# Kernel optimization log

Measured on AMD Instinct MI355X. Metric: run time of the kernel, lower is better.

Reference implementation:

```python
import jax, jax.numpy as jnp
import numpy as np


def _xnor_quant_weight(w):
    # XnorBinaryLinear.quant_weight: row-center, sign-binarize, scale by
    # per-output-channel mean absolute value (STE in training; forward value
    # is sign(wc) * scale).
    wc = w - jnp.mean(w, axis=1, keepdims=True)          # [OC, IC]
    scale = jnp.mean(jnp.abs(wc), axis=1, keepdims=True)  # [OC, 1]
    return jnp.sign(wc) * scale


def setup_inputs() -> dict:
    key = jax.random.key(0)
    k1, k2, k3, k4 = jax.random.split(key, 4)
    OC = IC = 4096
    N_OUT = int(0.05 * IC)  # 204 outlier columns
    TOKENS = 4096
    x = jax.random.normal(k1, (TOKENS, IC), dtype=jnp.float32)
    weight = jax.random.normal(k2, (OC, IC), dtype=jnp.float32) * 0.02
    bias = jax.random.normal(k3, (OC,), dtype=jnp.float32) * 0.02
    outlier_weight = jax.random.normal(k4, (OC, N_OUT), dtype=jnp.float32) * 0.02
    outlier_columns_index = jnp.arange(N_OUT, dtype=jnp.int32)
    return {
        "x": x,
        "weight": weight,
        "bias": bias,
        "outlier_weight": outlier_weight,
        "outlier_columns_index": outlier_columns_index,
    }


def reference(x, weight, bias, outlier_weight, outlier_columns_index):
    # binarize_except_outliers: quantize dense weight, then overwrite the
    # outlier input-channel columns with the kept full-precision weights.
    wq = _xnor_quant_weight(weight)                      # [OC, IC]
    wq = wq.at[:, outlier_columns_index].set(outlier_weight)
    # F.linear(x, w, b) = x @ w.T + b
    return jnp.einsum("ti,oi->to", x, wq) + bias
```

## Files before the change

kernel.cpp:

```cpp
#include <hip/hip_runtime.h>

typedef __bf16 bf16;
typedef __bf16 bf16x8 __attribute__((ext_vector_type(8)));
typedef float  f32x4  __attribute__((ext_vector_type(4)));
typedef float  f32x16 __attribute__((ext_vector_type(16)));
typedef int    i32x4  __attribute__((ext_vector_type(4)));
typedef int    i32x16 __attribute__((ext_vector_type(16)));
typedef signed char i8;

#define OC_N   4096
#define IC_K   4096
#define TOKENS 4096
#define KC     256

__global__ __launch_bounds__(256) void prep_kernel(
    const float* __restrict__ w, const float* __restrict__ x,
    const float* __restrict__ ow, const int* __restrict__ idx,
    i8* __restrict__ wsgn, i8* __restrict__ xq,
    bf16* __restrict__ xo, bf16* __restrict__ wcorr,
    float* __restrict__ scale_arr, float* __restrict__ sx_arr, int n_out)
{
    __shared__ float red[8];
    const int row = blockIdx.x;
    const int t = threadIdx.x;
    const int lane = t & 63, wv = t >> 6;

    const float4* wr = (const float4*)(w + (size_t)row * IC_K);
    const float4* xr = (const float4*)(x + (size_t)row * IC_K);
    float4 v[4], u[4];
#pragma unroll
    for (int i = 0; i < 4; i++) v[i] = wr[i * 256 + t];
#pragma unroll
    for (int i = 0; i < 4; i++) u[i] = xr[i * 256 + t];

    float xg = 0.f, wg = 0.f, og = 0.f;
    if (t < n_out) {
        const int colg = idx[t];
        xg = x[(size_t)row * IC_K + colg];
        wg = w[(size_t)row * IC_K + colg];
        og = ow[(size_t)row * n_out + t];
    }

    float s = 0.f;
#pragma unroll
    for (int i = 0; i < 4; i++)
        s += v[i].x + v[i].y + v[i].z + v[i].w;
    for (int o = 32; o > 0; o >>= 1) s += __shfl_down(s, o, 64);
    if (lane == 0) red[wv] = s;
    __syncthreads();
    const float mean = (red[0] + red[1] + red[2] + red[3]) * (1.f / IC_K);

    float sa = 0.f;
#pragma unroll
    for (int i = 0; i < 4; i++) {
        sa += fabsf(v[i].x - mean) + fabsf(v[i].y - mean) +
              fabsf(v[i].z - mean) + fabsf(v[i].w - mean);
    }
    for (int o = 32; o > 0; o >>= 1) sa += __shfl_down(sa, o, 64);
    if (lane == 0) red[4 + wv] = sa;
    __syncthreads();
    const float scale = (red[4] + red[5] + red[6] + red[7]) * (1.f / IC_K);

    i8* srow = wsgn + (size_t)row * IC_K;
#pragma unroll
    for (int i = 0; i < 4; i++) {
        float c[4] = { v[i].x - mean, v[i].y - mean, v[i].z - mean, v[i].w - mean };
        char4 q;
        q.x = (i8)((c[0] > 0.f) - (c[0] < 0.f));
        q.y = (i8)((c[1] > 0.f) - (c[1] < 0.f));
        q.z = (i8)((c[2] > 0.f) - (c[2] < 0.f));
        q.w = (i8)((c[3] > 0.f) - (c[3] < 0.f));
        *(char4*)(srow + (size_t)(i * 256 + t) * 4) = q;
    }

    float mx = 0.f;
#pragma unroll
    for (int i = 0; i < 4; i++)
        mx = fmaxf(mx, fmaxf(fmaxf(fabsf(u[i].x), fabsf(u[i].y)),
                             fmaxf(fabsf(u[i].z), fabsf(u[i].w))));
    for (int o = 32; o > 0; o >>= 1) mx = fmaxf(mx, __shfl_down(mx, o, 64));
    if (lane == 0) red[wv] = mx;
    __syncthreads();
    const float maxv = fmaxf(fmaxf(red[0], red[1]), fmaxf(red[2], red[3]));
    const float inv = maxv > 0.f ? 127.f / maxv : 0.f;
    const float sxv = maxv > 0.f ? maxv * (1.f / 127.f) : 1.f;

    i8* xrow = xq + (size_t)row * IC_K;
#pragma unroll
    for (int i = 0; i < 4; i++) {
        char4 q;
        q.x = (i8)(int)rintf(u[i].x * inv);
        q.y = (i8)(int)rintf(u[i].y * inv);
        q.z = (i8)(int)rintf(u[i].z * inv);
        q.w = (i8)(int)rintf(u[i].w * inv);
        *(char4*)(xrow + (size_t)(i * 256 + t) * 4) = q;
    }
    if (t == 0) { scale_arr[row] = scale; sx_arr[row] = sxv; }

    if (t < n_out) {
        xo[(size_t)row * KC + t] = (bf16)xg;
        const float wc_ = wg - mean;
        const float sg = (wc_ > 0.f) ? 1.f : ((wc_ < 0.f) ? -1.f : 0.f);
        wcorr[(size_t)row * KC + t] = (bf16)(og - scale * sg);
    } else if (t < KC) {
        xo[(size_t)row * KC + t] = (bf16)0.f;
        wcorr[(size_t)row * KC + t] = (bf16)0.f;
    }
}

__device__ __forceinline__ void gload16(const void* g, void* l)
{
    __builtin_amdgcn_global_load_lds(
        (const __attribute__((address_space(1))) void*)g,
        (__attribute__((address_space(3))) void*)l, 16, 0, 0);
}

#define VMCNT(n) asm volatile("s_waitcnt vmcnt(" #n ")" ::: "memory")
#define SCHED0   __builtin_amdgcn_sched_barrier(0)
#define BAR      __builtin_amdgcn_s_barrier()

__global__ __launch_bounds__(512, 2) void gemm_kernel(
    const i8* __restrict__ A, const i8* __restrict__ B,
    const bf16* __restrict__ Axo, const bf16* __restrict__ Bwc,
    const float* __restrict__ sx, const float* __restrict__ scale,
    const float* __restrict__ bias, float* __restrict__ C)
{
    constexpr int K = IC_K, N = OC_N;
    __shared__ __align__(16) i8 ring[5][2][16384];

    const int tid  = threadIdx.x;
    const int lane = tid & 63;
    const int wave = tid >> 6;
    const int wm = wave >> 2, wn = wave & 3;
    const int m32 = lane & 31, kg = lane >> 5;

    const int bid = blockIdx.x;
    const int xcd = bid & 7, tix = bid >> 3;
    const int bm = (xcd >> 1) * 4 + (tix & 3);
    const int bn = (xcd & 1) * 8 + (tix >> 2);

    const int Q0 = tid, Q1 = 512 + tid;
    const int r0 = Q0 >> 2, r1 = Q1 >> 2;
    const int q0 = (Q0 & 3) ^ ((r0 >> 1) & 3);
    const int q1 = (Q1 & 3) ^ ((r1 >> 1) & 3);
    const int d0 = Q0 * 16, d1 = Q1 * 16;

    const i8* gA0 = A + (size_t)(bm * 256 + r0) * K + q0 * 16;
    const i8* gA1 = A + (size_t)(bm * 256 + r1) * K + q1 * 16;
    const i8* gB0 = B + (size_t)(bn * 256 + r0) * K + q0 * 16;
    const i8* gB1 = B + (size_t)(bn * 256 + r1) * K + q1 * 16;

    auto stage = [&](int c) {
        i8* bs = &ring[c % 5][0][0];
        const int ko = c * 64;
        gload16(gA0 + ko, bs + d0);
        gload16(gA1 + ko, bs + d1);
        gload16(gB0 + ko, bs + 16384 + d0);
        gload16(gB1 + ko, bs + 16384 + d1);
    };

    int offA[4][2], offB[2][2];
#pragma unroll
    for (int mi = 0; mi < 4; ++mi) {
        const int r = wm * 128 + mi * 32 + m32;
#pragma unroll
        for (int ks = 0; ks < 2; ++ks)
            offA[mi][ks] = r * 64 + ((ks * 2 + kg) ^ ((r >> 1) & 3)) * 16;
    }
#pragma unroll
    for (int ni = 0; ni < 2; ++ni) {
        const int r = wn * 64 + ni * 32 + m32;
#pragma unroll
        for (int ks = 0; ks < 2; ++ks)
            offB[ni][ks] = r * 64 + ((ks * 2 + kg) ^ ((r >> 1) & 3)) * 16;
    }

    i32x16 acc[4][2] = {};

    auto phase_i8 = [&](int c) {
        const i8* sA = &ring[c % 5][0][0];
        const i8* sB = sA + 16384;
        i32x4 af[4][2], bfr[2][2];
#pragma unroll
        for (int mi = 0; mi < 4; ++mi)
#pragma unroll
            for (int ks = 0; ks < 2; ++ks)
                af[mi][ks] = *(const i32x4*)(sA + offA[mi][ks]);
#pragma unroll
        for (int ni = 0; ni < 2; ++ni)
#pragma unroll
            for (int ks = 0; ks < 2; ++ks)
                bfr[ni][ks] = *(const i32x4*)(sB + offB[ni][ks]);
        __builtin_amdgcn_s_setprio(1);
#pragma unroll
        for (int ks = 0; ks < 2; ++ks)
#pragma unroll
            for (int mi = 0; mi < 4; ++mi)
#pragma unroll
                for (int ni = 0; ni < 2; ++ni)
                    acc[mi][ni] = __builtin_amdgcn_mfma_i32_32x32x32_i8(
                        af[mi][ks], bfr[ni][ks], acc[mi][ni], 0, 0, 0);
        __builtin_amdgcn_s_setprio(0);
    };

    stage(0); stage(1); stage(2); stage(3);
#pragma unroll 5
    for (int c = 0; c < 60; ++c) {
        VMCNT(12); BAR; SCHED0;
        stage(c + 4);
        phase_i8(c);
    }
    VMCNT(12); BAR; SCHED0; phase_i8(60);
    VMCNT(8);  BAR; SCHED0; phase_i8(61);
    VMCNT(4);  BAR; SCHED0; phase_i8(62);
    VMCNT(0);  BAR; SCHED0; phase_i8(63);

    const int rbase = bm * 256 + wm * 128 + 4 * kg;
    const int cbase = bn * 256 + wn * 64 + m32;
    float scl2[2], bv2[2];
#pragma unroll
    for (int ni = 0; ni < 2; ++ni) {
        scl2[ni] = scale[cbase + ni * 32];
        bv2[ni]  = bias[cbase + ni * 32];
    }
    f32x16 facc[4][2];
#pragma unroll
    for (int mi = 0; mi < 4; ++mi)
#pragma unroll
        for (int r = 0; r < 16; ++r) {
            const float sxv = sx[rbase + mi * 32 + (r & 3) + 8 * (r >> 2)];
#pragma unroll
            for (int ni = 0; ni < 2; ++ni)
                facc[mi][ni][r] = (float)acc[mi][ni][r] * sxv * scl2[ni];
        }
    asm volatile("s_waitcnt vmcnt(0)" ::: "memory");
    BAR;

    const i8* cA0 = (const i8*)Axo + (size_t)(bm * 256 + r0) * (KC * 2) + q0 * 16;
    const i8* cA1 = (const i8*)Axo + (size_t)(bm * 256 + r1) * (KC * 2) + q1 * 16;
    const i8* cB0 = (const i8*)Bwc + (size_t)(bn * 256 + r0) * (KC * 2) + q0 * 16;
    const i8* cB1 = (const i8*)Bwc + (size_t)(bn * 256 + r1) * (KC * 2) + q1 * 16;
    auto stagec = [&](int c) {
        i8* bs = &ring[c % 5][0][0];
        const int ko = c * 64;
        gload16(cA0 + ko, bs + d0);
        gload16(cA1 + ko, bs + d1);
        gload16(cB0 + ko, bs + 16384 + d0);
        gload16(cB1 + ko, bs + 16384 + d1);
    };
    auto phase_bf = [&](int c) {
        const i8* sA = &ring[c % 5][0][0];
        const i8* sB = sA + 16384;
        bf16x8 af[4][2], bfr[2][2];
#pragma unroll
        for (int mi = 0; mi < 4; ++mi)
#pragma unroll
            for (int ks = 0; ks < 2; ++ks)
                af[mi][ks] = *(const bf16x8*)(sA + offA[mi][ks]);
#pragma unroll
        for (int ni = 0; ni < 2; ++ni)
#pragma unroll
            for (int ks = 0; ks < 2; ++ks)
                bfr[ni][ks] = *(const bf16x8*)(sB + offB[ni][ks]);
        __builtin_amdgcn_s_setprio(1);
#pragma unroll
        for (int ks = 0; ks < 2; ++ks)
#pragma unroll
            for (int mi = 0; mi < 4; ++mi)
#pragma unroll
                for (int ni = 0; ni < 2; ++ni)
                    facc[mi][ni] = __builtin_amdgcn_mfma_f32_32x32x16_bf16(
                        af[mi][ks], bfr[ni][ks], facc[mi][ni], 0, 0, 0);
        __builtin_amdgcn_s_setprio(0);
    };

    stagec(0); stagec(1); stagec(2);
#pragma unroll
    for (int c = 0; c < 5; ++c) {
        VMCNT(8); BAR; SCHED0;
        stagec(c + 3);
        phase_bf(c);
    }
    VMCNT(8); BAR; SCHED0; phase_bf(5);
    VMCNT(4); BAR; SCHED0; phase_bf(6);
    VMCNT(0); BAR; SCHED0; phase_bf(7);

#pragma unroll
    for (int mi = 0; mi < 4; ++mi)
#pragma unroll
        for (int r = 0; r < 16; ++r) {
            const int row = rbase + mi * 32 + (r & 3) + 8 * (r >> 2);
#pragma unroll
            for (int ni = 0; ni < 2; ++ni)
                C[(size_t)row * N + cbase + ni * 32] = facc[mi][ni][r] + bv2[ni];
        }
}

extern "C" void kernel_launch(void* const* d_in, const int* in_sizes, int n_in,
                              void* d_out, int out_size, void* d_ws, size_t ws_size,
                              hipStream_t stream)
{
    const float* x    = (const float*)d_in[0];
    const float* w    = (const float*)d_in[1];
    const float* bias = (const float*)d_in[2];
    const float* ow   = (const float*)d_in[3];
    const int*   idx  = (const int*)d_in[4];
    const int    n_out = in_sizes[4];
    float* out = (float*)d_out;

    char* ws = (char*)d_ws;
    i8*    xq    = (i8*)ws;
    i8*    wsgn  = (i8*)(ws + (size_t)16 * 1024 * 1024);
    bf16*  xo    = (bf16*)(ws + (size_t)32 * 1024 * 1024);
    bf16*  wcorr = (bf16*)(ws + (size_t)34 * 1024 * 1024);
    float* sx    = (float*)(ws + (size_t)36 * 1024 * 1024);
    float* scl   = (float*)(ws + (size_t)36 * 1024 * 1024 + 16 * 1024);

    hipLaunchKernelGGL(prep_kernel, dim3(OC_N), dim3(256), 0, stream,
                       w, x, ow, idx, wsgn, xq, xo, wcorr, scl, sx, n_out);
    hipLaunchKernelGGL(gemm_kernel, dim3(256), dim3(512), 0, stream,
                       xq, wsgn, xo, wcorr, sx, scl, bias, out);
}
```

Measured before the change: 252.6 us.

## Double-buffer LDS fragment registers to overlap shared reads with MFMA

Splits each K-phase into an LDS-read step and an MFMA step, with two register fragment sets (A/B) alternating. The reads for chunk c+1 are issued before the MFMAs for chunk c, so LDS latency hides behind matrix math. This applies to both the int8 main loop and the bf16 outlier correction loop, and the wait and barrier placement is adjusted to match. It doubles fragment register usage, which risks spills or lower occupancy, and the reworked ring-slot and vmcnt accounting must stay correct.

New measurement: 262.3 us. 3.9% more time.

```diff
diff --git a/kernel.cpp b/kernel.cpp
--- a/kernel.cpp
+++ b/kernel.cpp
@@ -177,10 +177,9 @@
 
     i32x16 acc[4][2] = {};
 
-    auto phase_i8 = [&](int c) {
+    auto reads_i8 = [&](int c, i32x4 (&af)[4][2], i32x4 (&bfr)[2][2]) {
         const i8* sA = &ring[c % 5][0][0];
         const i8* sB = sA + 16384;
-        i32x4 af[4][2], bfr[2][2];
 #pragma unroll
         for (int mi = 0; mi < 4; ++mi)
 #pragma unroll
@@ -191,6 +190,8 @@
 #pragma unroll
             for (int ks = 0; ks < 2; ++ks)
                 bfr[ni][ks] = *(const i32x4*)(sB + offB[ni][ks]);
+    };
+    auto mfma_i8 = [&](i32x4 (&af)[4][2], i32x4 (&bfr)[2][2]) {
         __builtin_amdgcn_s_setprio(1);
 #pragma unroll
         for (int ks = 0; ks < 2; ++ks)
@@ -203,17 +204,32 @@
         __builtin_amdgcn_s_setprio(0);
     };
 
+    i32x4 afA[4][2], bfrA[2][2], afB[4][2], bfrB[2][2];
+
     stage(0); stage(1); stage(2); stage(3);
-#pragma unroll 5
-    for (int c = 0; c < 60; ++c) {
-        VMCNT(12); BAR; SCHED0;
-        stage(c + 4);
-        phase_i8(c);
-    }
-    VMCNT(12); BAR; SCHED0; phase_i8(60);
-    VMCNT(8);  BAR; SCHED0; phase_i8(61);
-    VMCNT(4);  BAR; SCHED0; phase_i8(62);
-    VMCNT(0);  BAR; SCHED0; phase_i8(63);
+    VMCNT(8); BAR; SCHED0;
+    reads_i8(0, afA, bfrA);
+
+    for (int c = 0; c < 58; c += 2) {
+        stage(c + 4); SCHED0;
+        reads_i8(c + 1, afB, bfrB);
+        mfma_i8(afA, bfrA);
+        VMCNT(8); BAR; SCHED0;
+        stage(c + 5); SCHED0;
+        reads_i8(c + 2, afA, bfrA);
+        mfma_i8(afB, bfrB);
+        VMCNT(8); BAR; SCHED0;
+    }
+    stage(62); SCHED0; reads_i8(59, afB, bfrB); mfma_i8(afA, bfrA);
+    VMCNT(8); BAR; SCHED0;
+    stage(63); SCHED0; reads_i8(60, afA, bfrA); mfma_i8(afB, bfrB);
+    VMCNT(8); BAR; SCHED0;
+    reads_i8(61, afB, bfrB); mfma_i8(afA, bfrA);
+    VMCNT(4); BAR; SCHED0;
+    reads_i8(62, afA, bfrA); mfma_i8(afB, bfrB);
+    VMCNT(0); BAR; SCHED0;
+    reads_i8(63, afB, bfrB); mfma_i8(afA, bfrA);
+    mfma_i8(afB, bfrB);
 
     const int rbase = bm * 256 + wm * 128 + 4 * kg;
     const int cbase = bn * 256 + wn * 64 + m32;
@@ -248,10 +264,9 @@
         gload16(cB0 + ko, bs + 16384 + d0);
         gload16(cB1 + ko, bs + 16384 + d1);
     };
-    auto phase_bf = [&](int c) {
+    auto reads_bf = [&](int c, bf16x8 (&af)[4][2], bf16x8 (&bfr)[2][2]) {
         const i8* sA = &ring[c % 5][0][0];
         const i8* sB = sA + 16384;
-        bf16x8 af[4][2], bfr[2][2];
 #pragma unroll
         for (int mi = 0; mi < 4; ++mi)
 #pragma unroll
@@ -262,6 +277,8 @@
 #pragma unroll
             for (int ks = 0; ks < 2; ++ks)
                 bfr[ni][ks] = *(const bf16x8*)(sB + offB[ni][ks]);
+    };
+    auto mfma_bf = [&](bf16x8 (&af)[4][2], bf16x8 (&bfr)[2][2]) {
         __builtin_amdgcn_s_setprio(1);
 #pragma unroll
         for (int ks = 0; ks < 2; ++ks)
@@ -274,16 +291,27 @@
         __builtin_amdgcn_s_setprio(0);
     };
 
+    bf16x8 cfA[4][2], cgA[2][2], cfB[4][2], cgB[2][2];
     stagec(0); stagec(1); stagec(2);
-#pragma unroll
-    for (int c = 0; c < 5; ++c) {
-        VMCNT(8); BAR; SCHED0;
-        stagec(c + 3);
-        phase_bf(c);
-    }
-    VMCNT(8); BAR; SCHED0; phase_bf(5);
-    VMCNT(4); BAR; SCHED0; phase_bf(6);
-    VMCNT(0); BAR; SCHED0; phase_bf(7);
+    VMCNT(4); BAR; SCHED0;
+    reads_bf(0, cfA, cgA);
+
+    for (int c = 0; c < 4; c += 2) {
+        stagec(c + 3); SCHED0;
+        reads_bf(c + 1, cfB, cgB);
+        mfma_bf(cfA, cgA);
+        VMCNT(4); BAR; SCHED0;
+        stagec(c + 4); SCHED0;
+        reads_bf(c + 2, cfA, cgA);
+        mfma_bf(cfB, cgB);
+        VMCNT(4); BAR; SCHED0;
+    }
+    stagec(7); SCHED0; reads_bf(5, cfB, cgB); mfma_bf(cfA, cgA);
+    VMCNT(4); BAR; SCHED0;
+    reads_bf(6, cfA, cgA); mfma_bf(cfB, cgB);
+    VMCNT(0); BAR; SCHED0;
+    reads_bf(7, cfB, cgB); mfma_bf(cfA, cgA);
+    mfma_bf(cfB, cgB);
 
 #pragma unroll
     for (int mi = 0; mi < 4; ++mi)
```
